# Optimization experiments

Measured on AMD Instinct MI355X. Metric: run time of the kernel, lower is better.

## Reference

```python
import jax, jax.numpy as jnp
import numpy as np

B, C, H, W = 4, 256, 64, 64
CS = C // 2  # in_channels // scale_factor
EPS = 1e-5


def _conv1x1(x, w, b):
    # x: [B,C,H,W], w: [O,C], b: [O]
    return jnp.einsum('bchw,oc->bohw', x, w) + b[None, :, None, None]


def setup_inputs() -> dict:
    key = jax.random.key(0)
    ks = jax.random.split(key, 12)
    sq, so = 1.0 / np.sqrt(C), 1.0 / np.sqrt(CS)
    inp = {
        'input': jax.random.normal(ks[0], (B, C, H, W), jnp.float32),
        'Wq': jax.random.normal(ks[1], (CS, C), jnp.float32) * sq,
        'bq': jax.random.normal(ks[2], (CS,), jnp.float32) * 0.01,
        'Wk': jax.random.normal(ks[3], (CS, C), jnp.float32) * sq,
        'bk': jax.random.normal(ks[4], (CS,), jnp.float32) * 0.01,
        'Wv': jax.random.normal(ks[5], (CS, C), jnp.float32) * sq,
        'bv': jax.random.normal(ks[6], (CS,), jnp.float32) * 0.01,
        'Wo': jax.random.normal(ks[7], (C, CS), jnp.float32) * so,
        'bo': jax.random.normal(ks[8], (C,), jnp.float32) * 0.01,
        'gamma': 1.0 + 0.1 * jax.random.normal(ks[9], (C,), jnp.float32),
        'beta': 0.1 * jax.random.normal(ks[10], (C,), jnp.float32),
    }
    return inp


def reference(input, Wq, bq, Wk, bk, Wv, bv, Wo, bo, gamma, beta):
    b, c, w, h = input.shape
    n = w * h
    # 1x1-conv projections -> flattened spatial tokens
    q = _conv1x1(input, Wq, bq).reshape(b, CS, n).transpose(0, 2, 1)  # [B,N,CS]
    k = _conv1x1(input, Wk, bk).reshape(b, CS, n)                     # [B,CS,N]
    attn = jax.nn.softmax(jnp.matmul(q, k), axis=-1)                  # [B,N,N]
    v = _conv1x1(input, Wv, bv).reshape(b, CS, n).transpose(0, 2, 1)  # [B,N,CS]
    out = jnp.matmul(attn, v)                                         # [B,N,CS]
    out = out.transpose(0, 2, 1).reshape(b, CS, w, h)
    # output_conv: Conv2d(1x1) -> BatchNorm2d (training-mode batch stats) -> ReLU
    y = _conv1x1(out, Wo, bo)                                         # [B,C,H,W]
    mean = y.mean(axis=(0, 2, 3))
    var = y.var(axis=(0, 2, 3))  # biased, as torch BN normalization
    yn = (y - mean[None, :, None, None]) * jax.lax.rsqrt(var + EPS)[None, :, None, None]
    yn = yn * gamma[None, :, None, None] + beta[None, :, None, None]
    return jax.nn.relu(yn) + input
```

## Files before the change

kernel.cpp:

```cpp
#include <hip/hip_runtime.h>

#define NTOK 4096
#define NCH  256
#define NCS  128
#define NBAT 4

typedef _Float16 f16;
typedef _Float16 f16x8 __attribute__((ext_vector_type(8)));
typedef _Float16 f16x4 __attribute__((ext_vector_type(4)));
typedef __fp16 fp16x2 __attribute__((ext_vector_type(2)));
typedef float f32x16 __attribute__((ext_vector_type(16)));

__device__ __forceinline__ f16 f2h(float f) { return (f16)f; }
__device__ __forceinline__ float h2f(f16 h) { return (float)h; }
__device__ __forceinline__ unsigned short h2s(f16 h) {
  union { f16 h; unsigned short s; } u; u.h = h; return u.s;
}
__device__ __forceinline__ f32x16 mfma32(f16x8 a, f16x8 b, f32x16 c) {
  return __builtin_amdgcn_mfma_f32_32x32x16_f16(a, b, c, 0, 0, 0);
}
__device__ __forceinline__ unsigned pkrtz(float a, float b) {
  union { fp16x2 h; unsigned u; } u;
  u.h = __builtin_amdgcn_cvt_pkrtz(a, b);
  return u.u;
}

__global__ void k_wconv(const float* __restrict__ wq, const float* __restrict__ wk,
                        const float* __restrict__ wv, const float* __restrict__ wo,
                        f16* __restrict__ out) {
  int i = blockIdx.x * 256 + threadIdx.x;
  int seg = i >> 15, off = i & 32767;
  const float* s = (seg == 0) ? wq : (seg == 1) ? wk : (seg == 2) ? wv : wo;
  out[i] = f2h(s[off]);
}

__launch_bounds__(768)
__global__ void k_qkv(const float* __restrict__ x,
                      const f16* __restrict__ wqb, const f16* __restrict__ wkb,
                      const f16* __restrict__ wvb,
                      const float* __restrict__ bq, const float* __restrict__ bk,
                      const float* __restrict__ bv,
                      f16* __restrict__ Qt, f16* __restrict__ Kt, f16* __restrict__ Vc) {
  __shared__ f16 Xs[32][264];
  const int tid = threadIdx.x;
  const int b = blockIdx.y;
  const int t0 = blockIdx.x * 32;
  for (int idx = tid; idx < 4096; idx += 768) {
    const int tok = idx & 31, cp = idx >> 5;
    const float* xp = x + ((size_t)(b * NCH + 2 * cp)) * NTOK + t0 + tok;
    float f0 = xp[0];
    float f1 = xp[NTOK];
    unsigned pk = (unsigned)h2s(f2h(f0)) | ((unsigned)h2s(f2h(f1)) << 16);
    *(unsigned*)&Xs[tok][2 * cp] = pk;
  }
  __syncthreads();
  const int lane = tid & 63, w = tid >> 6;
  const int p = w >> 2, nt = w & 3;
  const int cc = lane & 31, hi = lane >> 5;
  const f16* wb = (p == 0) ? wqb : (p == 1) ? wkb : wvb;
  const float* bp = (p == 0) ? bq : (p == 1) ? bk : bv;

  f32x16 acc;
  #pragma unroll
  for (int i = 0; i < 16; i++) acc[i] = 0.f;
  #pragma unroll
  for (int ks = 0; ks < 16; ks++) {
    f16x8 a = *(const f16x8*)&Xs[cc][ks * 16 + hi * 8];
    f16x8 bw = *(const f16x8*)(wb + (size_t)(nt * 32 + cc) * NCH + ks * 16 + hi * 8);
    acc = mfma32(a, bw, acc);
  }
  const int oc = nt * 32 + cc;
  const float bias = bp[oc];
  if (p < 2) {
    f16* dst = (p == 0) ? Qt : Kt;
    #pragma unroll
    for (int i = 0; i < 16; i++) {
      int row = (i & 3) + 8 * (i >> 2) + 4 * hi;
      dst[((size_t)b * NTOK + t0 + row) * NCS + oc] = f2h(acc[i] + bias);
    }
  } else {
    #pragma unroll
    for (int q = 0; q < 4; q++) {
      f16x4 pk;
      #pragma unroll
      for (int j = 0; j < 4; j++) pk[j] = f2h(acc[4 * q + j] + bias);
      *(f16x4*)(Vc + ((size_t)b * NCS + oc) * NTOK + t0 + 8 * q + 4 * hi) = pk;
    }
  }
}

__launch_bounds__(256, 2)
__global__ void k_attn(const f16* __restrict__ Qt, const f16* __restrict__ Kt,
                       const f16* __restrict__ Vc,
                       f16* __restrict__ OP, float* __restrict__ ML, int niter) {
  __shared__ f16 Ks[2][64][136];
  __shared__ f16 Vs[2][128][72];
  __shared__ float als[4][32];
  const int tid = threadIdx.x;
  const int b = blockIdx.x & 3, kh = blockIdx.x >> 2, qt = blockIdx.y;
  const int lane = tid & 63, w = tid >> 6, cc = lane & 31, hi = lane >> 5;

  const f16* qp = Qt + ((size_t)b * NTOK + qt * 128 + w * 32 + cc) * NCS + hi * 8;
  f16x8 qf[8];
  #pragma unroll
  for (int ks = 0; ks < 8; ks++) qf[ks] = *(const f16x8*)(qp + ks * 16);

  f32x16 o[4];
  #pragma unroll
  for (int nt = 0; nt < 4; nt++)
    #pragma unroll
    for (int i = 0; i < 16; i++) o[nt][i] = 0.f;
  float m = -1e30f, l = 0.f;

  const int kkey = tid >> 2, kcb = (tid & 3) * 32;
  const int vd = tid >> 1, vh = (tid & 1) * 32;
  const int kb0 = kh * niter * 64;
  const f16* kbase = Kt + ((size_t)b * NTOK + kkey) * NCS + kcb;
  const f16* vbase = Vc + ((size_t)b * NCS + vd) * NTOK + vh;

  {
    const f16* kp = kbase + (size_t)kb0 * NCS;
    const f16* vp = vbase + kb0;
    #pragma unroll
    for (int pp = 0; pp < 4; pp++) {
      *(int4*)&Ks[0][kkey][kcb + pp * 8] = *(const int4*)(kp + pp * 8);
      *(int4*)&Vs[0][vd][vh + pp * 8] = *(const int4*)(vp + pp * 8);
    }
  }
  __syncthreads();

  for (int it = 0; it < niter; it++) {
    const int cur = it & 1;
    int4 kr0, kr1, kr2, kr3, vr0, vr1, vr2, vr3;
    const bool pf = (it + 1 < niter);
    if (pf) {
      const int kb = kb0 + (it + 1) * 64;
      const f16* kp = kbase + (size_t)kb * NCS;
      const f16* vp = vbase + kb;
      kr0 = *(const int4*)(kp);      kr1 = *(const int4*)(kp + 8);
      kr2 = *(const int4*)(kp + 16); kr3 = *(const int4*)(kp + 24);
      vr0 = *(const int4*)(vp);      vr1 = *(const int4*)(vp + 8);
      vr2 = *(const int4*)(vp + 16); vr3 = *(const int4*)(vp + 24);
    }

    f32x16 s0, s1;
    #pragma unroll
    for (int i = 0; i < 16; i++) { s0[i] = 0.f; s1[i] = 0.f; }
    #pragma unroll
    for (int ks = 0; ks < 8; ks++) {
      f16x8 a0 = *(const f16x8*)&Ks[cur][cc][ks * 16 + hi * 8];
      f16x8 a1 = *(const f16x8*)&Ks[cur][32 + cc][ks * 16 + hi * 8];
      s0 = mfma32(a0, qf[ks], s0);
      s1 = mfma32(a1, qf[ks], s1);
    }
    float t[16];
    #pragma unroll
    for (int i = 0; i < 16; i++) t[i] = fmaxf(s0[i], s1[i]);
    #pragma unroll
    for (int st = 8; st >= 1; st >>= 1)
      #pragma unroll
      for (int i = 0; i < st; i++) t[i] = fmaxf(t[i], t[i + st]);
    const float pmax = fmaxf(t[0], __shfl_xor(t[0], 32));

    if (__all(pmax <= m)) {
      float rs = 0.f;
      #pragma unroll
      for (int i = 0; i < 16; i++) { float e = __expf(s0[i] - m); s0[i] = e; rs += e; }
      #pragma unroll
      for (int i = 0; i < 16; i++) { float e = __expf(s1[i] - m); s1[i] = e; rs += e; }
      rs += __shfl_xor(rs, 32);
      l += rs;
    } else {
      const float mnew = fmaxf(m, pmax);
      const float alpha = __expf(m - mnew);
      float rs = 0.f;
      #pragma unroll
      for (int i = 0; i < 16; i++) { float e = __expf(s0[i] - mnew); s0[i] = e; rs += e; }
      #pragma unroll
      for (int i = 0; i < 16; i++) { float e = __expf(s1[i] - mnew); s1[i] = e; rs += e; }
      rs += __shfl_xor(rs, 32);
      l = l * alpha + rs;
      m = mnew;
      if (hi == 0) als[w][cc] = alpha;
      float ar[16];
      #pragma unroll
      for (int i = 0; i < 16; i++) ar[i] = als[w][(i & 3) + 8 * (i >> 2) + 4 * hi];
      #pragma unroll
      for (int nt = 0; nt < 4; nt++)
        #pragma unroll
        for (int i = 0; i < 16; i++) o[nt][i] *= ar[i];
    }

    f16x8 pav[4];
    {
      unsigned Wt[8];
      #pragma unroll
      for (int t2 = 0; t2 < 8; t2++) Wt[t2] = pkrtz(s0[2 * t2], s0[2 * t2 + 1]);
      asm volatile("v_permlane32_swap_b32 %0, %1" : "+v"(Wt[0]), "+v"(Wt[2]));
      asm volatile("v_permlane32_swap_b32 %0, %1" : "+v"(Wt[1]), "+v"(Wt[3]));
      asm volatile("v_permlane32_swap_b32 %0, %1" : "+v"(Wt[4]), "+v"(Wt[6]));
      asm volatile("v_permlane32_swap_b32 %0, %1" : "+v"(Wt[5]), "+v"(Wt[7]));
      union { unsigned u[4]; f16x8 v; } u0, u1;
      #pragma unroll
      for (int t2 = 0; t2 < 4; t2++) { u0.u[t2] = Wt[t2]; u1.u[t2] = Wt[4 + t2]; }
      pav[0] = u0.v; pav[1] = u1.v;
      #pragma unroll
      for (int t2 = 0; t2 < 8; t2++) Wt[t2] = pkrtz(s1[2 * t2], s1[2 * t2 + 1]);
      asm volatile("v_permlane32_swap_b32 %0, %1" : "+v"(Wt[0]), "+v"(Wt[2]));
      asm volatile("v_permlane32_swap_b32 %0, %1" : "+v"(Wt[1]), "+v"(Wt[3]));
      asm volatile("v_permlane32_swap_b32 %0, %1" : "+v"(Wt[4]), "+v"(Wt[6]));
      asm volatile("v_permlane32_swap_b32 %0, %1" : "+v"(Wt[5]), "+v"(Wt[7]));
      #pragma unroll
      for (int t2 = 0; t2 < 4; t2++) { u0.u[t2] = Wt[t2]; u1.u[t2] = Wt[4 + t2]; }
      pav[2] = u0.v; pav[3] = u1.v;
    }

    #pragma unroll
    for (int ks = 0; ks < 4; ks++) {
      #pragma unroll
      for (int nt = 0; nt < 4; nt++) {
        f16x8 bv = *(const f16x8*)&Vs[cur][nt * 32 + cc][ks * 16 + hi * 8];
        o[nt] = mfma32(pav[ks], bv, o[nt]);
      }
    }

    if (pf) {
      const int nxt = cur ^ 1;
      *(int4*)&Ks[nxt][kkey][kcb]      = kr0;
      *(int4*)&Ks[nxt][kkey][kcb + 8]  = kr1;
      *(int4*)&Ks[nxt][kkey][kcb + 16] = kr2;
      *(int4*)&Ks[nxt][kkey][kcb + 24] = kr3;
      *(int4*)&Vs[nxt][vd][vh]      = vr0;
      *(int4*)&Vs[nxt][vd][vh + 8]  = vr1;
      *(int4*)&Vs[nxt][vd][vh + 16] = vr2;
      *(int4*)&Vs[nxt][vd][vh + 24] = vr3;
    }
    __syncthreads();
  }
  const size_t obase = (((size_t)kh * NBAT + b) * NTOK + qt * 128 + w * 32);
  if (hi == 0) {
    const size_t mi = obase + cc;
    ML[mi * 2] = m; ML[mi * 2 + 1] = l;
  }
  #pragma unroll
  for (int nt = 0; nt < 4; nt++)
    #pragma unroll
    for (int i = 0; i < 16; i++) {
      int row = (i & 3) + 8 * (i >> 2) + 4 * hi;
      OP[(obase + row) * NCS + nt * 32 + cc] = f2h(o[nt][i]);
    }
}

template <int S>
__global__ void k_comb(const f16* __restrict__ OP, const float* __restrict__ ML,
                       f16* __restrict__ Oa) {
  const int gid = blockIdx.x * 256 + threadIdx.x;
  const int tok = gid >> 4, dg = (gid & 15) * 8;
  const int b = tok >> 12, tn = tok & 4095;
  float mv[S], lv[S];
  float mm = -1e30f;
  #pragma unroll
  for (int s = 0; s < S; s++) {
    const size_t idx = (((size_t)s * NBAT + b) * NTOK + tn);
    mv[s] = ML[idx * 2]; lv[s] = ML[idx * 2 + 1];
    mm = fmaxf(mm, mv[s]);
  }
  float den = 0.f, wsc[S];
  #pragma unroll
  for (int s = 0; s < S; s++) { wsc[s] = __expf(mv[s] - mm); den += wsc[s] * lv[s]; }
  const float inv = 1.f / den;
  float oacc[8];
  #pragma unroll
  for (int j = 0; j < 8; j++) oacc[j] = 0.f;
  #pragma unroll
  for (int s = 0; s < S; s++) {
    const size_t idx = (((size_t)s * NBAT + b) * NTOK + tn);
    int4 v = *(const int4*)(OP + idx * NCS + dg);
    const f16* a = (const f16*)&v;
    #pragma unroll
    for (int j = 0; j < 8; j++) oacc[j] += wsc[s] * h2f(a[j]);
  }
  f16x8 vv;
  #pragma unroll
  for (int j = 0; j < 8; j++) vv[j] = f2h(oacc[j] * inv);
  *(f16x8*)(Oa + ((size_t)b * NTOK + tn) * NCS + dg) = vv;
}

__launch_bounds__(256)
__global__ void k_out(const f16* __restrict__ Oa, const f16* __restrict__ wob,
                      const float* __restrict__ bo,
                      f16* __restrict__ Yb, float* __restrict__ Psum) {
  __shared__ f16 Es[256][72];
  const int tid = threadIdx.x;
  const int b = blockIdx.y, tt = blockIdx.x, t0 = tt * 64;
  const int lane = tid & 63, w = tid >> 6, cc = lane & 31, hi = lane >> 5;
  const int th = w >> 1, oh = w & 1;
  const f16* op = Oa + ((size_t)b * NTOK + t0 + th * 32 + cc) * NCS + hi * 8;
  f16x8 af[8];
  #pragma unroll
  for (int ks = 0; ks < 8; ks++) af[ks] = *(const f16x8*)(op + ks * 16);
  f32x16 acc[4];
  #pragma unroll
  for (int nt = 0; nt < 4; nt++)
    #pragma unroll
    for (int i = 0; i < 16; i++) acc[nt][i] = 0.f;
  #pragma unroll
  for (int ks = 0; ks < 8; ks++)
    #pragma unroll
    for (int nt = 0; nt < 4; nt++) {
      f16x8 bw = *(const f16x8*)(wob + (size_t)(oh * 128 + nt * 32 + cc) * NCS + ks * 16 + hi * 8);
      acc[nt] = mfma32(af[ks], bw, acc[nt]);
    }
  #pragma unroll
  for (int nt = 0; nt < 4; nt++) {
    const int co = oh * 128 + nt * 32 + cc;
    const float bias = bo[co];
    float s = 0.f, sq = 0.f;
    #pragma unroll
    for (int i = 0; i < 16; i++) {
      float v = acc[nt][i] + bias;
      acc[nt][i] = v; s += v; sq += v * v;
    }
    s += __shfl_xor(s, 32); sq += __shfl_xor(sq, 32);
    if (hi == 0) {
      const size_t pi = ((size_t)(b * 64 + tt) * 2 + th) * NCH + co;
      Psum[pi * 2] = s; Psum[pi * 2 + 1] = sq;
    }
    #pragma unroll
    for (int q = 0; q < 4; q++) {
      f16x4 pk;
      #pragma unroll
      for (int j = 0; j < 4; j++) pk[j] = f2h(acc[nt][4 * q + j]);
      *(f16x4*)&Es[co][th * 32 + q * 8 + hi * 4] = pk;
    }
  }
  __syncthreads();
  {
    const f16* er = &Es[tid][0];
    f16* yp = Yb + ((size_t)b * NCH + tid) * NTOK + t0;
    #pragma unroll
    for (int p = 0; p < 8; p++)
      *(int4*)(yp + p * 8) = *(const int4*)(er + p * 8);
  }
}

__global__ void k_stats(const float* __restrict__ Psum, float* __restrict__ St) {
  const int ch = blockIdx.x, tid = threadIdx.x;
  float s = 0.f, sq = 0.f;
  for (int i = tid; i < 512; i += 128) {
    s  += Psum[((size_t)i * NCH + ch) * 2];
    sq += Psum[((size_t)i * NCH + ch) * 2 + 1];
  }
  #pragma unroll
  for (int off = 32; off >= 1; off >>= 1) { s += __shfl_down(s, off); sq += __shfl_down(sq, off); }
  __shared__ float red[4];
  if ((tid & 63) == 0) { red[(tid >> 6) * 2] = s; red[(tid >> 6) * 2 + 1] = sq; }
  __syncthreads();
  if (tid == 0) {
    s = red[0] + red[2]; sq = red[1] + red[3];
    const float mean = s * (1.f / 16384.f);
    const float var = sq * (1.f / 16384.f) - mean * mean;
    St[ch * 2] = mean;
    St[ch * 2 + 1] = 1.f / sqrtf(var + 1e-5f);
  }
}

__global__ void k_final(const f16* __restrict__ Yb, const float* __restrict__ x,
                        const float* __restrict__ St, const float* __restrict__ gamma,
                        const float* __restrict__ beta, float* __restrict__ out) {
  const size_t i = ((size_t)blockIdx.x * 256 + threadIdx.x) * 8;
  const int ch = (int)((i >> 12) & 255);
  const float mean = St[ch * 2], rstd = St[ch * 2 + 1];
  const float sc = gamma[ch] * rstd;
  const float sh = beta[ch] - mean * sc;
  int4 yv = *(const int4*)(Yb + i);
  const f16* ys = (const f16*)&yv;
  const float4 x0 = *(const float4*)(x + i);
  const float4 x1 = *(const float4*)(x + i + 4);
  float4 o0, o1;
  o0.x = fmaxf(h2f(ys[0]) * sc + sh, 0.f) + x0.x;
  o0.y = fmaxf(h2f(ys[1]) * sc + sh, 0.f) + x0.y;
  o0.z = fmaxf(h2f(ys[2]) * sc + sh, 0.f) + x0.z;
  o0.w = fmaxf(h2f(ys[3]) * sc + sh, 0.f) + x0.w;
  o1.x = fmaxf(h2f(ys[4]) * sc + sh, 0.f) + x1.x;
  o1.y = fmaxf(h2f(ys[5]) * sc + sh, 0.f) + x1.y;
  o1.z = fmaxf(h2f(ys[6]) * sc + sh, 0.f) + x1.z;
  o1.w = fmaxf(h2f(ys[7]) * sc + sh, 0.f) + x1.w;
  *(float4*)(out + i) = o0;
  *(float4*)(out + i + 4) = o1;
}

extern "C" void kernel_launch(void* const* d_in, const int* in_sizes, int n_in,
                              void* d_out, int out_size, void* d_ws, size_t ws_size,
                              hipStream_t stream) {
  const float* x     = (const float*)d_in[0];
  const float* Wq    = (const float*)d_in[1];
  const float* bq    = (const float*)d_in[2];
  const float* Wk    = (const float*)d_in[3];
  const float* bk    = (const float*)d_in[4];
  const float* Wv    = (const float*)d_in[5];
  const float* bv    = (const float*)d_in[6];
  const float* Wo    = (const float*)d_in[7];
  const float* bo    = (const float*)d_in[8];
  const float* gamma = (const float*)d_in[9];
  const float* beta  = (const float*)d_in[10];
  float* out = (float*)d_out;
  char* ws = (char*)d_ws;

  const size_t OFF_W  = 0;
  const size_t OFF_QT = 262144;
  const size_t OFF_KT = OFF_QT + 4194304;
  const size_t OFF_VC = OFF_KT + 4194304;
  const size_t OFF_OP = OFF_VC + 4194304;
  const size_t opsz8 = (size_t)8 * NBAT * NTOK * NCS * 2;
  const size_t mlsz8 = (size_t)8 * NBAT * NTOK * 2 * 4;
  const size_t need8 = OFF_OP + opsz8 + mlsz8 + 1048576 + 4096;
  const int SPLIT = (ws_size >= need8) ? 8 : 4;
  const size_t opsz = (size_t)SPLIT * NBAT * NTOK * NCS * 2;
  const size_t mlsz = (size_t)SPLIT * NBAT * NTOK * 2 * 4;
  const size_t OFF_ML = OFF_OP + opsz;
  const size_t OFF_PS = OFF_ML + mlsz;
  const size_t OFF_ST = OFF_PS + 1048576;

  f16* wqb = (f16*)(ws + OFF_W);
  f16* wkb = (f16*)(ws + OFF_W + 65536);
  f16* wvb = (f16*)(ws + OFF_W + 131072);
  f16* wob = (f16*)(ws + OFF_W + 196608);
  f16* Qt  = (f16*)(ws + OFF_QT);
  f16* Kt  = (f16*)(ws + OFF_KT);
  f16* Vc  = (f16*)(ws + OFF_VC);
  f16* OP  = (f16*)(ws + OFF_OP);
  float* ML = (float*)(ws + OFF_ML);
  float* Psum = (float*)(ws + OFF_PS);
  float* St   = (float*)(ws + OFF_ST);
  f16* Yb = (f16*)(ws + OFF_QT);
  f16* Oa = (f16*)(ws + OFF_VC);

  k_wconv<<<512, 256, 0, stream>>>(Wq, Wk, Wv, Wo, wqb);
  k_qkv<<<dim3(128, 4), 768, 0, stream>>>(x, wqb, wkb, wvb, bq, bk, bv, Qt, Kt, Vc);
  k_attn<<<dim3(4 * SPLIT, 32), 256, 0, stream>>>(Qt, Kt, Vc, OP, ML, 64 / SPLIT);
  if (SPLIT == 8) k_comb<8><<<1024, 256, 0, stream>>>(OP, ML, Oa);
  else            k_comb<4><<<1024, 256, 0, stream>>>(OP, ML, Oa);
  k_out<<<dim3(64, 4), 256, 0, stream>>>(Oa, wob, bo, Yb, Psum);
  k_stats<<<256, 128, 0, stream>>>(Psum, St);
  k_final<<<2048, 256, 0, stream>>>(Yb, x, St, gamma, beta, out);
}
```

Measured before the change: 207.1 us.

## Fuse split-KV combine into output projection and fix split count at four

Removes the separate k_comb kernel and merges the flash-decoding partial outputs (log-sum-exp rescaling across splits) directly inside k_out while loading the A fragments. The KV split is hardcoded to 4 instead of choosing 8 when workspace allows. This drops one launch and the write/read of the combined attention output. In exchange, k_attn gets half as many blocks when 8 splits would have been chosen, each doing longer KV loops, and k_out does redundant combine work because two warps share each token row.

```diff
diff --git a/kernel.cpp b/kernel.cpp
--- a/kernel.cpp
+++ b/kernel.cpp
@@ -251,54 +251,46 @@
     }
 }
 
-template <int S>
-__global__ void k_comb(const f16* __restrict__ OP, const float* __restrict__ ML,
-                       f16* __restrict__ Oa) {
-  const int gid = blockIdx.x * 256 + threadIdx.x;
-  const int tok = gid >> 4, dg = (gid & 15) * 8;
-  const int b = tok >> 12, tn = tok & 4095;
-  float mv[S], lv[S];
-  float mm = -1e30f;
-  #pragma unroll
-  for (int s = 0; s < S; s++) {
-    const size_t idx = (((size_t)s * NBAT + b) * NTOK + tn);
-    mv[s] = ML[idx * 2]; lv[s] = ML[idx * 2 + 1];
-    mm = fmaxf(mm, mv[s]);
-  }
-  float den = 0.f, wsc[S];
-  #pragma unroll
-  for (int s = 0; s < S; s++) { wsc[s] = __expf(mv[s] - mm); den += wsc[s] * lv[s]; }
-  const float inv = 1.f / den;
-  float oacc[8];
-  #pragma unroll
-  for (int j = 0; j < 8; j++) oacc[j] = 0.f;
-  #pragma unroll
-  for (int s = 0; s < S; s++) {
-    const size_t idx = (((size_t)s * NBAT + b) * NTOK + tn);
-    int4 v = *(const int4*)(OP + idx * NCS + dg);
-    const f16* a = (const f16*)&v;
-    #pragma unroll
-    for (int j = 0; j < 8; j++) oacc[j] += wsc[s] * h2f(a[j]);
-  }
-  f16x8 vv;
-  #pragma unroll
-  for (int j = 0; j < 8; j++) vv[j] = f2h(oacc[j] * inv);
-  *(f16x8*)(Oa + ((size_t)b * NTOK + tn) * NCS + dg) = vv;
-}
-
 __launch_bounds__(256)
-__global__ void k_out(const f16* __restrict__ Oa, const f16* __restrict__ wob,
-                      const float* __restrict__ bo,
+__global__ void k_out(const f16* __restrict__ OP, const float* __restrict__ ML,
+                      const f16* __restrict__ wob, const float* __restrict__ bo,
                       f16* __restrict__ Yb, float* __restrict__ Psum) {
   __shared__ f16 Es[256][72];
   const int tid = threadIdx.x;
   const int b = blockIdx.y, tt = blockIdx.x, t0 = tt * 64;
   const int lane = tid & 63, w = tid >> 6, cc = lane & 31, hi = lane >> 5;
   const int th = w >> 1, oh = w & 1;
-  const f16* op = Oa + ((size_t)b * NTOK + t0 + th * 32 + cc) * NCS + hi * 8;
+  const int tok = t0 + th * 32 + cc;
+
+  float mv[4], lv[4], mm = -1e30f;
+  #pragma unroll
+  for (int s = 0; s < 4; s++) {
+    const size_t idx = ((size_t)(s * NBAT + b) * NTOK + tok);
+    mv[s] = ML[idx * 2]; lv[s] = ML[idx * 2 + 1];
+    mm = fmaxf(mm, mv[s]);
+  }
+  float den = 0.f, wsc[4];
+  #pragma unroll
+  for (int s = 0; s < 4; s++) { wsc[s] = __expf(mv[s] - mm); den += wsc[s] * lv[s]; }
+  const float inv = 1.f / den;
+
   f16x8 af[8];
   #pragma unroll
-  for (int ks = 0; ks < 8; ks++) af[ks] = *(const f16x8*)(op + ks * 16);
+  for (int ks = 0; ks < 8; ks++) {
+    float oacc[8];
+    #pragma unroll
+    for (int j = 0; j < 8; j++) oacc[j] = 0.f;
+    #pragma unroll
+    for (int s = 0; s < 4; s++) {
+      int4 v = *(const int4*)(OP + ((size_t)(s * NBAT + b) * NTOK + tok) * NCS + ks * 16 + hi * 8);
+      const f16* a = (const f16*)&v;
+      #pragma unroll
+      for (int j = 0; j < 8; j++) oacc[j] += wsc[s] * h2f(a[j]);
+    }
+    #pragma unroll
+    for (int j = 0; j < 8; j++) af[ks][j] = f2h(oacc[j] * inv);
+  }
+
   f32x16 acc[4];
   #pragma unroll
   for (int nt = 0; nt < 4; nt++)
@@ -412,12 +404,8 @@
   const size_t OFF_KT = OFF_QT + 4194304;
   const size_t OFF_VC = OFF_KT + 4194304;
   const size_t OFF_OP = OFF_VC + 4194304;
-  const size_t opsz8 = (size_t)8 * NBAT * NTOK * NCS * 2;
-  const size_t mlsz8 = (size_t)8 * NBAT * NTOK * 2 * 4;
-  const size_t need8 = OFF_OP + opsz8 + mlsz8 + 1048576 + 4096;
-  const int SPLIT = (ws_size >= need8) ? 8 : 4;
-  const size_t opsz = (size_t)SPLIT * NBAT * NTOK * NCS * 2;
-  const size_t mlsz = (size_t)SPLIT * NBAT * NTOK * 2 * 4;
+  const size_t opsz = (size_t)4 * NBAT * NTOK * NCS * 2;
+  const size_t mlsz = (size_t)4 * NBAT * NTOK * 2 * 4;
   const size_t OFF_ML = OFF_OP + opsz;
   const size_t OFF_PS = OFF_ML + mlsz;
   const size_t OFF_ST = OFF_PS + 1048576;
@@ -434,14 +422,11 @@
   float* Psum = (float*)(ws + OFF_PS);
   float* St   = (float*)(ws + OFF_ST);
   f16* Yb = (f16*)(ws + OFF_QT);
-  f16* Oa = (f16*)(ws + OFF_VC);
 
   k_wconv<<<512, 256, 0, stream>>>(Wq, Wk, Wv, Wo, wqb);
   k_qkv<<<dim3(128, 4), 768, 0, stream>>>(x, wqb, wkb, wvb, bq, bk, bv, Qt, Kt, Vc);
-  k_attn<<<dim3(4 * SPLIT, 32), 256, 0, stream>>>(Qt, Kt, Vc, OP, ML, 64 / SPLIT);
-  if (SPLIT == 8) k_comb<8><<<1024, 256, 0, stream>>>(OP, ML, Oa);
-  else            k_comb<4><<<1024, 256, 0, stream>>>(OP, ML, Oa);
-  k_out<<<dim3(64, 4), 256, 0, stream>>>(Oa, wob, bo, Yb, Psum);
+  k_attn<<<dim3(16, 32), 256, 0, stream>>>(Qt, Kt, Vc, OP, ML, 16);
+  k_out<<<dim3(64, 4), 256, 0, stream>>>(OP, ML, wob, bo, Yb, Psum);
   k_stats<<<256, 128, 0, stream>>>(Psum, St);
   k_final<<<2048, 256, 0, stream>>>(Yb, x, St, gamma, beta, out);
 }
```

New measurement: 199.5 us. -3.7%, faster.
